# Optimization experiments

Measured on AMD Instinct MI355X. Metric: run time of the kernel, lower is better.

## Reference

```python
import jax, jax.numpy as jnp
import numpy as np

DIM = 512
T = 65536


def setup_inputs() -> dict:
    key = jax.random.key(0)
    k1, = jax.random.split(key, 1)
    z_rest = jax.random.normal(k1, (T, DIM), dtype=jnp.float32)
    # var_vbl = inv_softplus(sqrt(var_init)) with var_init=1.0 -> log(expm1(1.0))
    var_vbl = jnp.full((DIM,), float(np.log(np.expm1(1.0))), dtype=jnp.float32)
    # corr_vbl = inv_sigmoid(0.1) = log(0.1) - log(0.9)
    corr_vbl = jnp.full((DIM,), float(np.log(0.1) - np.log(0.9)), dtype=jnp.float32)
    prior_mu = jnp.zeros((DIM,), dtype=jnp.float32)
    return {"z_rest": z_rest, "var_vbl": var_vbl, "corr_vbl": corr_vbl, "prior_mu": prior_mu}


def reference(z_rest, var_vbl, corr_vbl, prior_mu):
    # init_train_lkd with z_context=None, starting from fresh state (sample_size=0).
    prior_var = jnp.square(jax.nn.softplus(var_vbl))          # [D]
    prior_cov = jax.nn.sigmoid(corr_vbl) * prior_var          # [D]
    two_pi = 2.0 * jnp.pi

    def step(carry, xs):
        mu, var, lkd = carry
        z, t = xs  # z: [D], t: scalar step index (== sample_size - 1 after increment)
        lkd = lkd + jnp.sum(-0.5 * jnp.log(two_pi * var)
                            - jnp.square(z - mu) / (2.0 * var))
        dd = prior_cov / (prior_var + prior_cov * t)
        mu = (1.0 - dd) * mu + z * dd
        var = (1.0 - dd) * var + (prior_var - prior_cov) * dd
        return (mu, var, lkd), None

    ts = jnp.arange(z_rest.shape[0], dtype=z_rest.dtype)
    init = (prior_mu.astype(z_rest.dtype), prior_var, jnp.zeros((), z_rest.dtype))
    (_, _, lkd), _ = jax.lax.scan(step, init, (z_rest, ts))
    return lkd
```

## Files before the change

kernel.cpp:

```cpp
#include <hip/hip_runtime.h>
#include <math.h>


#define DIM    512
#define TT     65536
#define CHUNKS 1024
#define ROWS   64
#define GROUPS 64
#define CPG    16

#define TWO_PI 6.283185307179586

__global__ __launch_bounds__(256) void k1_colsum(const float* __restrict__ z,
                                                 float* __restrict__ sums) {
    const int chunk = blockIdx.x;
    const int c2 = threadIdx.x;
    const float2* zp = reinterpret_cast<const float2*>(z)
                       + (size_t)chunk * ROWS * (DIM / 2) + c2;
    float sx = 0.f, sy = 0.f;
#pragma unroll 16
    for (int r = 0; r < ROWS; ++r) {
        float2 v = zp[(size_t)r * (DIM / 2)];
        sx += v.x;
        sy += v.y;
    }
    float2* sp = reinterpret_cast<float2*>(sums) + (size_t)chunk * (DIM / 2) + c2;
    *sp = make_float2(sx, sy);
}

__global__ __launch_bounds__(512) void k2a_scan(float* __restrict__ sums,
                                                float* __restrict__ gsums) {
    const int g = blockIdx.x;
    const int d = threadIdx.x;
    float run = 0.f;
#pragma unroll
    for (int i = 0; i < CPG; ++i) {
        const size_t idx = (size_t)(g * CPG + i) * DIM + d;
        float t = sums[idx];
        sums[idx] = run;
        run += t;
    }
    gsums[(size_t)g * DIM + d] = run;
}

__global__ __launch_bounds__(512) void k2b_scan(float* __restrict__ gsums,
                                                const float* __restrict__ var_vbl,
                                                const float* __restrict__ corr_vbl,
                                                float* __restrict__ out) {
    const int d = threadIdx.x;
    float run = 0.f;
#pragma unroll 16
    for (int g = 0; g < GROUPS; ++g) {
        float t = gsums[(size_t)g * DIM + d];
        gsums[(size_t)g * DIM + d] = run;
        run += t;
    }
    double sp = log1p(exp((double)var_vbl[d]));
    double v = sp * sp;
    double cc = v / (1.0 + exp(-(double)corr_vbl[d]));
    double vmc = v - cc;
    double Dlast = v + cc * (double)(TT - 1);
    double Ld = -0.5 * ((double)TT * (log(TWO_PI) + log(vmc)) + log(Dlast / vmc));
    __shared__ double red[512];
    red[d] = Ld;
    __syncthreads();
    for (int s = 256; s > 0; s >>= 1) {
        if (d < s) red[d] += red[d + s];
        __syncthreads();
    }
    if (d == 0) atomicAdd(out, (float)red[0]);
}

__global__ __launch_bounds__(256) void k3_main(const float* __restrict__ z,
                                               const float* __restrict__ sums,
                                               const float* __restrict__ gsums,
                                               const float* __restrict__ var_vbl,
                                               const float* __restrict__ corr_vbl,
                                               const float* __restrict__ prior_mu,
                                               float* __restrict__ out) {
    const int chunk = blockIdx.x;
    const int tid = threadIdx.x;
    const int d0 = tid * 2;
    const int g = chunk / CPG;
    const float t0m1 = (float)(chunk * ROWS) - 1.0f;

    float vv[2], cc[2], k0[2], kq[2], Z[2], Dprev[2], invDprev[2];
#pragma unroll
    for (int j = 0; j < 2; ++j) {
        const int d = d0 + j;
        float spv = log1pf(expf(var_vbl[d]));
        float v = spv * spv;
        float c = v / (1.0f + expf(-corr_vbl[d]));
        float vmc = v - c;
        vv[j] = v;
        cc[j] = c;
        k0[j] = vmc * prior_mu[d];
        kq[j] = 0.5f / vmc;
        Z[j] = sums[(size_t)chunk * DIM + d] + gsums[(size_t)g * DIM + d];
        Dprev[j] = fmaf(c, t0m1, v);
        invDprev[j] = __builtin_amdgcn_rcpf(Dprev[j]);
    }

    const float2* zp = reinterpret_cast<const float2*>(z)
                       + (size_t)chunk * ROWS * (DIM / 2) + tid;
    float acc = 0.f;
    float tf = t0m1 + 1.0f;
#pragma unroll 4
    for (int r = 0; r < ROWS; ++r) {
        float2 zv = zp[(size_t)r * (DIM / 2)];
        float zz[2] = {zv.x, zv.y};
#pragma unroll
        for (int j = 0; j < 2; ++j) {
            float Dt = fmaf(cc[j], tf, vv[j]);
            float invDt = __builtin_amdgcn_rcpf(Dt);
            float mu = fmaf(cc[j], Z[j], k0[j]) * invDprev[j];
            float e = zz[j] - mu;
            acc = fmaf(e * e * Dprev[j] * invDt, kq[j], acc);
            Z[j] += zz[j];
            Dprev[j] = Dt;
            invDprev[j] = invDt;
        }
        tf += 1.0f;
    }

    for (int off = 32; off > 0; off >>= 1) acc += __shfl_down(acc, off, 64);
    __shared__ float wsred[4];
    const int lane = tid & 63, w = tid >> 6;
    if (lane == 0) wsred[w] = acc;
    __syncthreads();
    if (tid == 0) atomicAdd(out, -(wsred[0] + wsred[1] + wsred[2] + wsred[3]));
}

extern "C" void kernel_launch(void* const* d_in, const int* in_sizes, int n_in,
                              void* d_out, int out_size, void* d_ws, size_t ws_size,
                              hipStream_t stream) {
    const float* z = (const float*)d_in[0];
    const float* var_vbl = (const float*)d_in[1];
    const float* corr_vbl = (const float*)d_in[2];
    const float* prior_mu = (const float*)d_in[3];
    float* out = (float*)d_out;
    float* sums = (float*)d_ws;
    float* gsums = sums + (size_t)CHUNKS * DIM;

    hipMemsetAsync(d_out, 0, sizeof(float), stream);
    k1_colsum<<<CHUNKS, 256, 0, stream>>>(z, sums);
    k2a_scan<<<GROUPS, 512, 0, stream>>>(sums, gsums);
    k2b_scan<<<1, 512, 0, stream>>>(gsums, var_vbl, corr_vbl, out);
    k3_main<<<CHUNKS, 256, 0, stream>>>(z, sums, gsums, var_vbl, corr_vbl,
                                        prior_mu, out);
}
```

Before: 233.1 us.

## Use float4 loads, smaller row chunks, and drop output memset

Switches both the column-sum and main kernels to 128-thread blocks that load float4 per thread, handling four columns each. Rows per chunk are halved so twice as many chunks are launched, which keeps the block count high. The memset of the output is removed; the scan kernel now writes the output directly and the main kernel still accumulates into it with atomics. The intent is wider memory transactions and one fewer launch, at the cost of doubling the scan workspace and the number of atomics.

```diff
diff --git a/kernel.cpp b/kernel.cpp
--- a/kernel.cpp
+++ b/kernel.cpp
@@ -4,28 +4,27 @@
 
 #define DIM    512
 #define TT     65536
-#define CHUNKS 1024
-#define ROWS   64
+#define CHUNKS 2048
+#define ROWS   32
 #define GROUPS 64
-#define CPG    16
+#define CPG    32
 
 #define TWO_PI 6.283185307179586
 
-__global__ __launch_bounds__(256) void k1_colsum(const float* __restrict__ z,
+__global__ __launch_bounds__(128) void k1_colsum(const float* __restrict__ z,
                                                  float* __restrict__ sums) {
     const int chunk = blockIdx.x;
-    const int c2 = threadIdx.x;
-    const float2* zp = reinterpret_cast<const float2*>(z)
-                       + (size_t)chunk * ROWS * (DIM / 2) + c2;
-    float sx = 0.f, sy = 0.f;
-#pragma unroll 16
+    const int t = threadIdx.x;
+    const float4* zp = reinterpret_cast<const float4*>(z)
+                       + (size_t)chunk * ROWS * (DIM / 4) + t;
+    float sx = 0.f, sy = 0.f, sz = 0.f, sw = 0.f;
+#pragma unroll 8
     for (int r = 0; r < ROWS; ++r) {
-        float2 v = zp[(size_t)r * (DIM / 2)];
-        sx += v.x;
-        sy += v.y;
+        float4 v = zp[(size_t)r * (DIM / 4)];
+        sx += v.x; sy += v.y; sz += v.z; sw += v.w;
     }
-    float2* sp = reinterpret_cast<float2*>(sums) + (size_t)chunk * (DIM / 2) + c2;
-    *sp = make_float2(sx, sy);
+    float4* sp = reinterpret_cast<float4*>(sums) + (size_t)chunk * (DIM / 4) + t;
+    *sp = make_float4(sx, sy, sz, sw);
 }
 
 __global__ __launch_bounds__(512) void k2a_scan(float* __restrict__ sums,
@@ -33,7 +32,7 @@
     const int g = blockIdx.x;
     const int d = threadIdx.x;
     float run = 0.f;
-#pragma unroll
+#pragma unroll 8
     for (int i = 0; i < CPG; ++i) {
         const size_t idx = (size_t)(g * CPG + i) * DIM + d;
         float t = sums[idx];
@@ -49,7 +48,7 @@
                                                 float* __restrict__ out) {
     const int d = threadIdx.x;
     float run = 0.f;
-#pragma unroll 16
+#pragma unroll 8
     for (int g = 0; g < GROUPS; ++g) {
         float t = gsums[(size_t)g * DIM + d];
         gsums[(size_t)g * DIM + d] = run;
@@ -68,10 +67,10 @@
         if (d < s) red[d] += red[d + s];
         __syncthreads();
     }
-    if (d == 0) atomicAdd(out, (float)red[0]);
+    if (d == 0) out[0] = (float)red[0];
 }
 
-__global__ __launch_bounds__(256) void k3_main(const float* __restrict__ z,
+__global__ __launch_bounds__(128) void k3_main(const float* __restrict__ z,
                                                const float* __restrict__ sums,
                                                const float* __restrict__ gsums,
                                                const float* __restrict__ var_vbl,
@@ -80,13 +79,13 @@
                                                float* __restrict__ out) {
     const int chunk = blockIdx.x;
     const int tid = threadIdx.x;
-    const int d0 = tid * 2;
+    const int d0 = tid * 4;
     const int g = chunk / CPG;
     const float t0m1 = (float)(chunk * ROWS) - 1.0f;
 
-    float vv[2], cc[2], k0[2], kq[2], Z[2], Dprev[2], invDprev[2];
+    float vv[4], cc[4], k0[4], kq[4], Z[4], Dprev[4], invDprev[4];
 #pragma unroll
-    for (int j = 0; j < 2; ++j) {
+    for (int j = 0; j < 4; ++j) {
         const int d = d0 + j;
         float spv = log1pf(expf(var_vbl[d]));
         float v = spv * spv;
@@ -101,16 +100,16 @@
         invDprev[j] = __builtin_amdgcn_rcpf(Dprev[j]);
     }
 
-    const float2* zp = reinterpret_cast<const float2*>(z)
-                       + (size_t)chunk * ROWS * (DIM / 2) + tid;
+    const float4* zp = reinterpret_cast<const float4*>(z)
+                       + (size_t)chunk * ROWS * (DIM / 4) + tid;
     float acc = 0.f;
     float tf = t0m1 + 1.0f;
 #pragma unroll 4
     for (int r = 0; r < ROWS; ++r) {
-        float2 zv = zp[(size_t)r * (DIM / 2)];
-        float zz[2] = {zv.x, zv.y};
+        float4 zv = zp[(size_t)r * (DIM / 4)];
+        float zz[4] = {zv.x, zv.y, zv.z, zv.w};
 #pragma unroll
-        for (int j = 0; j < 2; ++j) {
+        for (int j = 0; j < 4; ++j) {
             float Dt = fmaf(cc[j], tf, vv[j]);
             float invDt = __builtin_amdgcn_rcpf(Dt);
             float mu = fmaf(cc[j], Z[j], k0[j]) * invDprev[j];
@@ -124,11 +123,11 @@
     }
 
     for (int off = 32; off > 0; off >>= 1) acc += __shfl_down(acc, off, 64);
-    __shared__ float wsred[4];
+    __shared__ float wsred[2];
     const int lane = tid & 63, w = tid >> 6;
     if (lane == 0) wsred[w] = acc;
     __syncthreads();
-    if (tid == 0) atomicAdd(out, -(wsred[0] + wsred[1] + wsred[2] + wsred[3]));
+    if (tid == 0) atomicAdd(out, -(wsred[0] + wsred[1]));
 }
 
 extern "C" void kernel_launch(void* const* d_in, const int* in_sizes, int n_in,
@@ -142,10 +141,9 @@
     float* sums = (float*)d_ws;
     float* gsums = sums + (size_t)CHUNKS * DIM;
 
-    hipMemsetAsync(d_out, 0, sizeof(float), stream);
-    k1_colsum<<<CHUNKS, 256, 0, stream>>>(z, sums);
+    k1_colsum<<<CHUNKS, 128, 0, stream>>>(z, sums);
     k2a_scan<<<GROUPS, 512, 0, stream>>>(sums, gsums);
     k2b_scan<<<1, 512, 0, stream>>>(gsums, var_vbl, corr_vbl, out);
-    k3_main<<<CHUNKS, 256, 0, stream>>>(z, sums, gsums, var_vbl, corr_vbl,
+    k3_main<<<CHUNKS, 128, 0, stream>>>(z, sums, gsums, var_vbl, corr_vbl,
                                         prior_mu, out);
 }
```

After: 242.5 us. +4.0%, slower.
